# Performance work log

Hardware: AMD Instinct MI355X
Metric: run time of the kernel (lower is better)

## Reference

```python
import jax, jax.numpy as jnp
import numpy as np

CODEBOOK_SIZE = 32768
EMBED_DIM = 32
BETA = 0.25


def setup_inputs() -> dict:
    key = jax.random.key(0)
    k_z, k_cb = jax.random.split(key)
    z = jax.random.normal(k_z, (4, EMBED_DIM, 32, 32), dtype=jnp.float32)
    codebook = jax.random.normal(k_cb, (CODEBOOK_SIZE, EMBED_DIM), dtype=jnp.float32)
    return {"z": z, "codebook": codebook}


def reference(z, codebook):
    # z: [B, C, H, W] -> flatten to [N, C] tokens (channel-last, as in torch VQ)
    B, C, H, W = z.shape
    zf = jnp.transpose(z, (0, 2, 3, 1)).reshape(-1, C)  # [N, C]
    # squared L2 distance to every code: ||z||^2 - 2 z.e + ||e||^2  -> [N, K]
    d = (
        jnp.sum(zf * zf, axis=-1, keepdims=True)
        - 2.0 * (zf @ codebook.T)
        + jnp.sum(codebook * codebook, axis=-1)[None, :]
    )
    idx = jnp.argmin(d, axis=-1)  # [N]
    zq = codebook[idx].reshape(B, H, W, C).transpose(0, 3, 1, 2)  # [B, C, H, W]
    # codebook + commitment losses
    loss = jnp.mean((jax.lax.stop_gradient(zq) - z) ** 2) + BETA * jnp.mean(
        (zq - jax.lax.stop_gradient(z)) ** 2
    )
    # straight-through estimator
    zq_st = z + jax.lax.stop_gradient(zq - z)
    return zq_st, loss
```

## Files before the change

kernel.cpp:

```cpp
#include <hip/hip_runtime.h>
#include <math.h>

#define K_CB    32768
#define C_DIM   32
#define N_TOK   4096
#define OUT_N   (N_TOK * C_DIM)

#define SLICES  64
#define KPERSL  (K_CB / SLICES)
#define GROUPS  (KPERSL / 16)
#define SCALE   4096.0f

typedef _Float16 half8   __attribute__((ext_vector_type(8)));
typedef float    floatx4 __attribute__((ext_vector_type(4)));

__global__ __launch_bounds__(256) void vq_prep(const float* __restrict__ z,
                                               const float* __restrict__ cb,
                                               _Float16* __restrict__ zh,
                                               _Float16* __restrict__ zl,
                                               _Float16* __restrict__ ch,
                                               _Float16* __restrict__ cl,
                                               float* __restrict__ nrm,
                                               float* __restrict__ out) {
    const int bb = blockIdx.x;
    if (bb < 128) {
        const int k = bb * 256 + threadIdx.x;
        const float4* src = (const float4*)(cb + (size_t)k * C_DIM);
        _Float16 h[C_DIM], l[C_DIM];
        float s = 0.f;
#pragma unroll
        for (int i = 0; i < 8; ++i) {
            float4 v = src[i];
            s = fmaf(v.x, v.x, s); s = fmaf(v.y, v.y, s);
            s = fmaf(v.z, v.z, s); s = fmaf(v.w, v.w, s);
            float x[4] = {v.x * SCALE, v.y * SCALE, v.z * SCALE, v.w * SCALE};
#pragma unroll
            for (int j = 0; j < 4; ++j) {
                _Float16 hh = (_Float16)x[j];
                h[i * 4 + j] = hh;
                l[i * 4 + j] = (_Float16)(x[j] - (float)hh);
            }
        }
        nrm[k] = s;
        half8* dh = (half8*)(ch + (size_t)k * C_DIM);
        half8* dl = (half8*)(cl + (size_t)k * C_DIM);
#pragma unroll
        for (int i = 0; i < 4; ++i) {
            dh[i] = *(half8*)&h[i * 8];
            dl[i] = *(half8*)&l[i * 8];
        }
        if (k == 0) out[OUT_N] = 0.f;
    } else {
        const int tok = (bb - 128) * 256 + threadIdx.x;
        const int b = tok >> 10, hw = tok & 1023;
        const float* zp = z + (size_t)b * (C_DIM * 1024) + hw;
        _Float16 h[C_DIM], l[C_DIM];
#pragma unroll
        for (int c = 0; c < C_DIM; ++c) {
            float xs = zp[(size_t)c * 1024] * SCALE;
            _Float16 hh = (_Float16)xs;
            h[c] = hh;
            l[c] = (_Float16)(xs - (float)hh);
        }
        half8* dh = (half8*)(zh + (size_t)tok * C_DIM);
        half8* dl = (half8*)(zl + (size_t)tok * C_DIM);
#pragma unroll
        for (int i = 0; i < 4; ++i) {
            dh[i] = *(half8*)&h[i * 8];
            dl[i] = *(half8*)&l[i * 8];
        }
    }
}

__global__ __launch_bounds__(256) void vq_mfma(const _Float16* __restrict__ zh,
                                               const _Float16* __restrict__ zl,
                                               const _Float16* __restrict__ ch,
                                               const _Float16* __restrict__ cl,
                                               const float* __restrict__ nrm,
                                               unsigned long long* __restrict__ keys) {
    const int tid   = threadIdx.x;
    const int lane  = tid & 63, wid = tid >> 6;
    const int row16 = lane & 15, kgrp = lane >> 4;
    const int tile  = blockIdx.x & 15;
    const int slice = blockIdx.x >> 4;
    const int tokA  = tile * 256 + wid * 64 + row16;
    const int code0 = slice * KPERSL;

    half8 ah[4], al[4];
#pragma unroll
    for (int s = 0; s < 4; ++s) {
        ah[s] = *(const half8*)(zh + (size_t)(tokA + s * 16) * C_DIM + kgrp * 8);
        al[s] = *(const half8*)(zl + (size_t)(tokA + s * 16) * C_DIM + kgrp * 8);
    }

    const _Float16* pbh = ch + (size_t)(code0 + row16) * C_DIM + kgrp * 8;
    const _Float16* pbl = cl + (size_t)(code0 + row16) * C_DIM + kgrp * 8;
    const float*    pn  = nrm + code0 + row16;
    int kc = code0 + row16;

    float best[4][4]; int bk[4][4];
#pragma unroll
    for (int s = 0; s < 4; ++s)
#pragma unroll
        for (int j = 0; j < 4; ++j) { best[s][j] = -INFINITY; bk[s][j] = 0; }

    for (int g = 0; g < GROUPS; ++g) {
        half8 bh = *(const half8*)pbh;
        half8 bl = *(const half8*)pbl;
        float initv = (*pn) * -8388608.0f;
        floatx4 acc[4];
#pragma unroll
        for (int s = 0; s < 4; ++s) {
            acc[s] = (floatx4){initv, initv, initv, initv};
            acc[s] = __builtin_amdgcn_mfma_f32_16x16x32_f16(ah[s], bl, acc[s], 0, 0, 0);
            acc[s] = __builtin_amdgcn_mfma_f32_16x16x32_f16(al[s], bh, acc[s], 0, 0, 0);
            acc[s] = __builtin_amdgcn_mfma_f32_16x16x32_f16(ah[s], bh, acc[s], 0, 0, 0);
        }
#pragma unroll
        for (int s = 0; s < 4; ++s)
#pragma unroll
            for (int j = 0; j < 4; ++j) {
                float v = acc[s][j];
                bool gt = v > best[s][j];
                best[s][j] = gt ? v : best[s][j];
                bk[s][j]   = gt ? kc : bk[s][j];
            }
        pbh += 16 * C_DIM; pbl += 16 * C_DIM; pn += 16; kc += 16;
    }

#pragma unroll
    for (int off = 1; off < 16; off <<= 1)
#pragma unroll
        for (int s = 0; s < 4; ++s)
#pragma unroll
            for (int j = 0; j < 4; ++j) {
                float os = __shfl_xor(best[s][j], off, 64);
                int   ok = __shfl_xor(bk[s][j],   off, 64);
                bool t = (os > best[s][j]) || (os == best[s][j] && ok < bk[s][j]);
                best[s][j] = t ? os : best[s][j];
                bk[s][j]   = t ? ok : bk[s][j];
            }

    if (row16 == 0) {
#pragma unroll
        for (int s = 0; s < 4; ++s)
#pragma unroll
            for (int j = 0; j < 4; ++j) {
                int t0 = tile * 256 + wid * 64 + s * 16 + kgrp * 4 + j;
                float d = best[s][j] * -1.1920928955078125e-7f;
                unsigned u = __float_as_uint(d);
                u ^= (u & 0x80000000u) ? 0xFFFFFFFFu : 0x80000000u;
                unsigned long long key =
                    ((unsigned long long)u << 32) | (unsigned)bk[s][j];
                atomicMin(keys + t0, key);
            }
    }
}

__global__ __launch_bounds__(256) void vq_finalize(const float* __restrict__ z,
                                                   const float* __restrict__ cb,
                                                   const unsigned long long* __restrict__ keys,
                                                   float* __restrict__ out) {
    const int tok0 = blockIdx.x * 32;
    const int b = tok0 >> 10, hw0 = tok0 & 1023;
    const int tt = threadIdx.x & 31;
    const int sq = threadIdx.x >> 5;
    const int tok = tok0 + tt;

    const int k  = (int)(keys[tok] & 0xFFFFFFFFu);
    const int c0 = sq * 4;
    float4 e = *(const float4*)(cb + (size_t)k * C_DIM + c0);
    float ev[4] = {e.x, e.y, e.z, e.w};

    const float* zp = z   + (size_t)b * (C_DIM * 1024) + hw0 + tt;
    float*       op = out + (size_t)b * (C_DIM * 1024) + hw0 + tt;
    float lsum = 0.f;
#pragma unroll
    for (int j = 0; j < 4; ++j) {
        float zc = zp[(size_t)(c0 + j) * 1024];
        float df = ev[j] - zc;
        lsum = fmaf(df, df, lsum);
        op[(size_t)(c0 + j) * 1024] = ev[j];
    }

#pragma unroll
    for (int off = 32; off > 0; off >>= 1) lsum += __shfl_down(lsum, off, 64);
    __shared__ float wsum[4];
    const int lane = threadIdx.x & 63, wid = threadIdx.x >> 6;
    if (lane == 0) wsum[wid] = lsum;
    __syncthreads();
    if (threadIdx.x == 0)
        atomicAdd(out + OUT_N, (wsum[0] + wsum[1] + wsum[2] + wsum[3]) * (1.25f / (float)OUT_N));
}

extern "C" void kernel_launch(void* const* d_in, const int* in_sizes, int n_in,
                              void* d_out, int out_size, void* d_ws, size_t ws_size,
                              hipStream_t stream) {
    const float* z  = (const float*)d_in[0];
    const float* cb = (const float*)d_in[1];
    float* out = (float*)d_out;

    _Float16* zh = (_Float16*)d_ws;
    _Float16* zl = zh + (size_t)N_TOK * C_DIM;
    _Float16* ch = zl + (size_t)N_TOK * C_DIM;
    _Float16* cl = ch + (size_t)K_CB * C_DIM;
    float*  norms = (float*)(cl + (size_t)K_CB * C_DIM);
    unsigned long long* keys = (unsigned long long*)(norms + K_CB);

    hipMemsetAsync(keys, 0xFF, (size_t)N_TOK * 8, stream);
    vq_prep    <<<144, 256, 0, stream>>>(z, cb, zh, zl, ch, cl, norms, out);
    vq_mfma    <<<(N_TOK / 256) * SLICES, 256, 0, stream>>>(zh, zl, ch, cl, norms, keys);
    vq_finalize<<<N_TOK / 32, 256, 0, stream>>>(z, cb, keys, out);
}
```

Measured before the change: 121.7 us.

## Halve per-wave token tile, prefetch codebook loads, fold key init into prep

Each wave of the distance kernel now covers 32 tokens instead of 64, and the grid doubles to 2048 blocks. This cuts live registers and raises occupancy, at the cost of loading each codebook fragment twice as often. The codebook fragment and norm loads are software-pipelined one group ahead to hide global memory latency behind the MFMAs. The separate memset of the argmin keys is removed and done inside the prep kernel, saving one launch.

Result: faster. 117.3 us (-3.6%).

```diff
diff --git a/kernel.cpp b/kernel.cpp
--- a/kernel.cpp
+++ b/kernel.cpp
@@ -21,6 +21,7 @@
                                                _Float16* __restrict__ ch,
                                                _Float16* __restrict__ cl,
                                                float* __restrict__ nrm,
+                                               unsigned long long* __restrict__ keys,
                                                float* __restrict__ out) {
     const int bb = blockIdx.x;
     if (bb < 128) {
@@ -69,6 +70,7 @@
             dh[i] = *(half8*)&h[i * 8];
             dl[i] = *(half8*)&l[i * 8];
         }
+        keys[tok] = 0xFFFFFFFFFFFFFFFFull;
     }
 }
 
@@ -81,79 +83,96 @@
     const int tid   = threadIdx.x;
     const int lane  = tid & 63, wid = tid >> 6;
     const int row16 = lane & 15, kgrp = lane >> 4;
-    const int tile  = blockIdx.x & 15;
-    const int slice = blockIdx.x >> 4;
-    const int tokA  = tile * 256 + wid * 64 + row16;
+    const int tile  = blockIdx.x & 31;
+    const int slice = blockIdx.x >> 5;
+    const int tokA  = tile * 128 + wid * 32 + row16;
     const int code0 = slice * KPERSL;
 
-    half8 ah[4], al[4];
-#pragma unroll
-    for (int s = 0; s < 4; ++s) {
-        ah[s] = *(const half8*)(zh + (size_t)(tokA + s * 16) * C_DIM + kgrp * 8);
-        al[s] = *(const half8*)(zl + (size_t)(tokA + s * 16) * C_DIM + kgrp * 8);
-    }
+    const half8 a0h = *(const half8*)(zh + (size_t)tokA * C_DIM + kgrp * 8);
+    const half8 a0l = *(const half8*)(zl + (size_t)tokA * C_DIM + kgrp * 8);
+    const half8 a1h = *(const half8*)(zh + (size_t)(tokA + 16) * C_DIM + kgrp * 8);
+    const half8 a1l = *(const half8*)(zl + (size_t)(tokA + 16) * C_DIM + kgrp * 8);
 
     const _Float16* pbh = ch + (size_t)(code0 + row16) * C_DIM + kgrp * 8;
     const _Float16* pbl = cl + (size_t)(code0 + row16) * C_DIM + kgrp * 8;
     const float*    pn  = nrm + code0 + row16;
     int kc = code0 + row16;
 
-    float best[4][4]; int bk[4][4];
-#pragma unroll
-    for (int s = 0; s < 4; ++s)
-#pragma unroll
-        for (int j = 0; j < 4; ++j) { best[s][j] = -INFINITY; bk[s][j] = 0; }
-
-    for (int g = 0; g < GROUPS; ++g) {
-        half8 bh = *(const half8*)pbh;
-        half8 bl = *(const half8*)pbl;
-        float initv = (*pn) * -8388608.0f;
-        floatx4 acc[4];
-#pragma unroll
-        for (int s = 0; s < 4; ++s) {
-            acc[s] = (floatx4){initv, initv, initv, initv};
-            acc[s] = __builtin_amdgcn_mfma_f32_16x16x32_f16(ah[s], bl, acc[s], 0, 0, 0);
-            acc[s] = __builtin_amdgcn_mfma_f32_16x16x32_f16(al[s], bh, acc[s], 0, 0, 0);
-            acc[s] = __builtin_amdgcn_mfma_f32_16x16x32_f16(ah[s], bh, acc[s], 0, 0, 0);
-        }
-#pragma unroll
-        for (int s = 0; s < 4; ++s)
-#pragma unroll
-            for (int j = 0; j < 4; ++j) {
-                float v = acc[s][j];
-                bool gt = v > best[s][j];
-                best[s][j] = gt ? v : best[s][j];
-                bk[s][j]   = gt ? kc : bk[s][j];
-            }
-        pbh += 16 * C_DIM; pbl += 16 * C_DIM; pn += 16; kc += 16;
-    }
+    float best0[4], best1[4]; int bk0[4], bk1[4];
+#pragma unroll
+    for (int j = 0; j < 4; ++j) {
+        best0[j] = -INFINITY; best1[j] = -INFINITY; bk0[j] = 0; bk1[j] = 0;
+    }
+
+    half8 bh = *(const half8*)pbh;
+    half8 bl = *(const half8*)pbl;
+    float nv = *pn;
+
+#define VQ_STEP(BH, BL, NV)                                                    \
+    {                                                                          \
+        float initv = (NV) * -8388608.0f;                   \
+        floatx4 acc0 = {initv, initv, initv, initv};                           \
+        floatx4 acc1 = acc0;                                                   \
+        acc0 = __builtin_amdgcn_mfma_f32_16x16x32_f16(a0h, (BL), acc0, 0,0,0); \
+        acc1 = __builtin_amdgcn_mfma_f32_16x16x32_f16(a1h, (BL), acc1, 0,0,0); \
+        acc0 = __builtin_amdgcn_mfma_f32_16x16x32_f16(a0l, (BH), acc0, 0,0,0); \
+        acc1 = __builtin_amdgcn_mfma_f32_16x16x32_f16(a1l, (BH), acc1, 0,0,0); \
+        acc0 = __builtin_amdgcn_mfma_f32_16x16x32_f16(a0h, (BH), acc0, 0,0,0); \
+        acc1 = __builtin_amdgcn_mfma_f32_16x16x32_f16(a1h, (BH), acc1, 0,0,0); \
+        _Pragma("unroll")                                                      \
+        for (int j = 0; j < 4; ++j) {     \
+            float v0 = acc0[j];                                                \
+            bool g0 = v0 > best0[j];                                           \
+            best0[j] = g0 ? v0 : best0[j];                                     \
+            bk0[j]   = g0 ? kc : bk0[j];                                       \
+            float v1 = acc1[j];                                                \
+            bool g1 = v1 > best1[j];                                           \
+            best1[j] = g1 ? v1 : best1[j];                                     \
+            bk1[j]   = g1 ? kc : bk1[j];                                       \
+        }                                                                      \
+    }
+
+    for (int g = 0; g < GROUPS - 1; ++g) {
+        pbh += 16 * C_DIM; pbl += 16 * C_DIM; pn += 16;
+        half8 nbh = *(const half8*)pbh;
+        half8 nbl = *(const half8*)pbl;
+        float nnv = *pn;
+        VQ_STEP(bh, bl, nv)
+        bh = nbh; bl = nbl; nv = nnv; kc += 16;
+    }
+    VQ_STEP(bh, bl, nv)
+#undef VQ_STEP
 
 #pragma unroll
     for (int off = 1; off < 16; off <<= 1)
 #pragma unroll
-        for (int s = 0; s < 4; ++s)
-#pragma unroll
-            for (int j = 0; j < 4; ++j) {
-                float os = __shfl_xor(best[s][j], off, 64);
-                int   ok = __shfl_xor(bk[s][j],   off, 64);
-                bool t = (os > best[s][j]) || (os == best[s][j] && ok < bk[s][j]);
-                best[s][j] = t ? os : best[s][j];
-                bk[s][j]   = t ? ok : bk[s][j];
-            }
+        for (int j = 0; j < 4; ++j) {
+            float os = __shfl_xor(best0[j], off, 64);
+            int   ok = __shfl_xor(bk0[j],   off, 64);
+            bool t = (os > best0[j]) || (os == best0[j] && ok < bk0[j]);
+            best0[j] = t ? os : best0[j];
+            bk0[j]   = t ? ok : bk0[j];
+            os = __shfl_xor(best1[j], off, 64);
+            ok = __shfl_xor(bk1[j],   off, 64);
+            t = (os > best1[j]) || (os == best1[j] && ok < bk1[j]);
+            best1[j] = t ? os : best1[j];
+            bk1[j]   = t ? ok : bk1[j];
+        }
 
     if (row16 == 0) {
 #pragma unroll
-        for (int s = 0; s < 4; ++s)
-#pragma unroll
-            for (int j = 0; j < 4; ++j) {
-                int t0 = tile * 256 + wid * 64 + s * 16 + kgrp * 4 + j;
-                float d = best[s][j] * -1.1920928955078125e-7f;
+        for (int j = 0; j < 4; ++j) {
+#pragma unroll
+            for (int s = 0; s < 2; ++s) {
+                int t0 = tile * 128 + wid * 32 + s * 16 + kgrp * 4 + j;
+                float d = (s ? best1[j] : best0[j]) * -1.1920928955078125e-7f;
                 unsigned u = __float_as_uint(d);
                 u ^= (u & 0x80000000u) ? 0xFFFFFFFFu : 0x80000000u;
                 unsigned long long key =
-                    ((unsigned long long)u << 32) | (unsigned)bk[s][j];
+                    ((unsigned long long)u << 32) | (unsigned)(s ? bk1[j] : bk0[j]);
                 atomicMin(keys + t0, key);
             }
+        }
     }
 }
 
@@ -207,8 +226,7 @@
     float*  norms = (float*)(cl + (size_t)K_CB * C_DIM);
     unsigned long long* keys = (unsigned long long*)(norms + K_CB);
 
-    hipMemsetAsync(keys, 0xFF, (size_t)N_TOK * 8, stream);
-    vq_prep    <<<144, 256, 0, stream>>>(z, cb, zh, zl, ch, cl, norms, out);
-    vq_mfma    <<<(N_TOK / 256) * SLICES, 256, 0, stream>>>(zh, zl, ch, cl, norms, keys);
+    vq_prep    <<<144, 256, 0, stream>>>(z, cb, zh, zl, ch, cl, norms, keys, out);
+    vq_mfma    <<<(N_TOK / 128) * SLICES, 256, 0, stream>>>(zh, zl, ch, cl, norms, keys);
     vq_finalize<<<N_TOK / 32, 256, 0, stream>>>(z, cb, keys, out);
 }
```
